# Kernel tuning notes

Measured on AMD Instinct MI355X. Metric: run time of the kernel, lower is better.

## Reference

```python
import jax, jax.numpy as jnp
import numpy as np

K = 256
ALPHA = 0.2   # bml_alpha
BETA = 0.3    # bml_beta
EPS = 1e-8    # torch CosineSimilarity eps
NEG_INF = -10000.0
WEIGHT_TEMP = 0.05


def _l2n(x):
    # cosine-normalize rows, matching nn.CosineSimilarity's eps clamp
    n = jnp.linalg.norm(x, axis=-1, keepdims=True)
    return x / jnp.maximum(n, EPS)


def setup_inputs() -> dict:
    key = jax.random.key(0)
    k1, k2, k3 = jax.random.split(key, 3)
    B, D = 8192, 768
    datapoints = jax.random.normal(k1, (B, D), dtype=jnp.float32)
    centroid = jax.random.normal(k2, (K, D), dtype=jnp.float32)
    batch_cos_sim = jax.random.normal(k3, (B, B), dtype=jnp.float32)
    return {"datapoints": datapoints, "centroid": centroid, "batch_cos_sim": batch_cos_sim}


def reference(datapoints, centroid, batch_cos_sim):
    B = datapoints.shape[0]
    datapoints = jax.lax.stop_gradient(datapoints)  # forward() does clone().detach()

    # intra_cos_sim = cos(datapoints, centroid) / temp (temp=1)  -> [B, K]
    intra_cos_sim = _l2n(datapoints) @ _l2n(centroid).T

    # cluster assignment + intra-class adjacency
    dp_index = jnp.argmax(intra_cos_sim, axis=-1)                 # [B]
    onehot = jax.nn.one_hot(dp_index, K, dtype=jnp.float32)       # [B, K]
    dp_cluster = onehot @ onehot.T                                # [B, B]
    eye = jnp.eye(B, dtype=bool)
    dp_cluster = jnp.where(eye, 0.0, dp_cluster)                  # fill_diagonal_(0)

    # gather assigned centroid per datapoint
    dp_centroid = centroid[dp_index]                              # [B, D]

    # hard negative: 2nd-closest centroid (top-2 on cosine sim), detached
    _, top2_idx = jax.lax.top_k(intra_cos_sim, 2)                 # [B, 2]
    hard_negative = jax.lax.stop_gradient(centroid[top2_idx[:, 1]])  # [B, D]

    # false-negative BML loss on the in-batch cosine matrix
    pos = jnp.diagonal(batch_cos_sim)[:, None]                    # [B, 1]
    delta = (batch_cos_sim - pos) * dp_cluster                    # [B, B]
    fn_loss = (jax.nn.relu(delta + ALPHA) + jax.nn.relu(-delta - BETA)).mean()

    # softmax-weighted negatives (diag masked to -10000), detached
    masked = jnp.where(eye, NEG_INF, batch_cos_sim)
    weights = jax.lax.stop_gradient(jax.nn.softmax(masked, axis=-1) / WEIGHT_TEMP)

    return intra_cos_sim, dp_cluster, dp_centroid, hard_negative, fn_loss, weights
```

## Files before the change

### kernel.cpp

```cpp
#include <hip/hip_runtime.h>
#include <math.h>

#define B_N 8192
#define K_N 256
#define D_N 768
#define BM 32
#define KC 32

static constexpr float ALPHA_C = 0.2f;
static constexpr float BETA_C  = 0.3f;
static constexpr float EPS_C   = 1e-8f;
static constexpr float NEG_INF_C = -10000.0f;
static constexpr float INV_WTEMP = 20.0f;

__global__ __launch_bounds__(256) void k_centroid_prep(
        const float* __restrict__ centroid, float* __restrict__ cnt) {
    int c = blockIdx.x, t = threadIdx.x;
    const float* p = centroid + c * D_N;
    float v0 = p[t], v1 = p[t + 256], v2 = p[t + 512];
    float s = v0 * v0 + v1 * v1 + v2 * v2;
    #pragma unroll
    for (int o = 32; o >= 1; o >>= 1) s += __shfl_xor(s, o);
    __shared__ float red[4];
    __shared__ float sinv;
    if ((t & 63) == 0) red[t >> 6] = s;
    __syncthreads();
    if (t == 0)
        sinv = 1.0f / fmaxf(sqrtf(red[0] + red[1] + red[2] + red[3]), EPS_C);
    __syncthreads();
    float inv = sinv;
    cnt[(t)       * K_N + c] = v0 * inv;
    cnt[(t + 256) * K_N + c] = v1 * inv;
    cnt[(t + 512) * K_N + c] = v2 * inv;
}

__device__ __forceinline__ bool top_better(float v, int iv, float w, int iw) {
    return (v > w) || ((v == w) && (iv < iw));
}

__global__ __launch_bounds__(256) void k_intra(
        const float* __restrict__ dp, const float* __restrict__ cnt,
        const float* __restrict__ centroid,
        float* __restrict__ out_intra, unsigned char* __restrict__ cid_g,
        float* __restrict__ dp_centroid, float* __restrict__ hard_negative) {
    __shared__ float ct[KC][K_N];
    __shared__ float dpt[KC][BM + 4];
    __shared__ float sqp[BM][8];
    __shared__ float rn[BM];
    int t = threadIdx.x;
    int row0 = blockIdx.x * BM;
    int tx = t & 63, ty = t >> 6;
    int c0 = tx * 4;
    int r0 = ty * 8;
    int sr = t >> 3, skq = t & 7;

    float acc[8][4];
    #pragma unroll
    for (int r = 0; r < 8; ++r)
        #pragma unroll
        for (int c = 0; c < 4; ++c) acc[r][c] = 0.f;
    float ss = 0.f;

    for (int kb = 0; kb < D_N; kb += KC) {
        __syncthreads();
        #pragma unroll
        for (int u = 0; u < 8; ++u) {
            int f4 = t + 256 * u;
            int k = f4 >> 6, c4 = (f4 & 63) << 2;
            *(float4*)&ct[k][c4] = *(const float4*)&cnt[(size_t)(kb + k) * K_N + c4];
        }
        {
            float4 v = *(const float4*)&dp[(size_t)(row0 + sr) * D_N + kb + skq * 4];
            ss += v.x * v.x + v.y * v.y + v.z * v.z + v.w * v.w;
            dpt[skq * 4 + 0][sr] = v.x;
            dpt[skq * 4 + 1][sr] = v.y;
            dpt[skq * 4 + 2][sr] = v.z;
            dpt[skq * 4 + 3][sr] = v.w;
        }
        __syncthreads();
        #pragma unroll
        for (int k = 0; k < KC; ++k) {
            float4 b4 = *(float4*)&ct[k][c0];
            float4 a0 = *(float4*)&dpt[k][r0];
            float4 a1 = *(float4*)&dpt[k][r0 + 4];
            float a[8] = {a0.x, a0.y, a0.z, a0.w, a1.x, a1.y, a1.z, a1.w};
            float b[4] = {b4.x, b4.y, b4.z, b4.w};
            #pragma unroll
            for (int r = 0; r < 8; ++r)
                #pragma unroll
                for (int c = 0; c < 4; ++c)
                    acc[r][c] += a[r] * b[c];
        }
    }

    sqp[sr][skq] = ss;
    __syncthreads();
    if (t < BM) {
        float s = 0.f;
        #pragma unroll
        for (int j = 0; j < 8; ++j) s += sqp[t][j];
        rn[t] = 1.0f / fmaxf(sqrtf(s), EPS_C);
    }
    __syncthreads();

    #pragma unroll 1
    for (int r = 0; r < 8; ++r) {
        int row = row0 + r0 + r;
        float rv = rn[r0 + r];
        float4 o;
        o.x = acc[r][0] * rv; o.y = acc[r][1] * rv;
        o.z = acc[r][2] * rv; o.w = acc[r][3] * rv;
        *(float4*)&out_intra[(size_t)row * K_N + c0] = o;

        float m1 = o.x, m2 = -1e30f;
        int i1 = c0, i2 = K_N;
        { float v = o.y; int id = c0 + 1;
          if (v > m1) { m2 = m1; i2 = i1; m1 = v; i1 = id; } else if (v > m2) { m2 = v; i2 = id; } }
        { float v = o.z; int id = c0 + 2;
          if (v > m1) { m2 = m1; i2 = i1; m1 = v; i1 = id; } else if (v > m2) { m2 = v; i2 = id; } }
        { float v = o.w; int id = c0 + 3;
          if (v > m1) { m2 = m1; i2 = i1; m1 = v; i1 = id; } else if (v > m2) { m2 = v; i2 = id; } }
        #pragma unroll
        for (int off = 32; off >= 1; off >>= 1) {
            float om1 = __shfl_xor(m1, off);
            int   oi1 = __shfl_xor(i1, off);
            float om2 = __shfl_xor(m2, off);
            int   oi2 = __shfl_xor(i2, off);
            if (top_better(om1, oi1, m1, i1)) {
                if (top_better(m1, i1, om2, oi2)) { m2 = m1; i2 = i1; }
                else                              { m2 = om2; i2 = oi2; }
                m1 = om1; i1 = oi1;
            } else if (top_better(om1, oi1, m2, i2)) {
                m2 = om1; i2 = oi1;
            }
        }
        if (tx == 0) cid_g[row] = (unsigned char)i1;

        const float4* s1 = (const float4*)(centroid + (size_t)i1 * D_N);
        const float4* s2 = (const float4*)(centroid + (size_t)i2 * D_N);
        float4* d1 = (float4*)(dp_centroid   + (size_t)row * D_N);
        float4* d2 = (float4*)(hard_negative + (size_t)row * D_N);
        #pragma unroll
        for (int u = 0; u < 3; ++u) {
            d1[tx + 64 * u] = s1[tx + 64 * u];
            d2[tx + 64 * u] = s2[tx + 64 * u];
        }
    }
}

__global__ __launch_bounds__(256) void k_row(
        const float* __restrict__ bcs, const unsigned char* __restrict__ cid_g,
        float* __restrict__ dp_cluster, float* __restrict__ weights,
        float* __restrict__ partials) {
    int i = blockIdx.x;
    int t = threadIdx.x;
    __shared__ float red_se[4], red_fn[4];
    __shared__ float posb;
    const unsigned* cidw = (const unsigned*)cid_g;

    const float4* src = (const float4*)(bcs + (size_t)i * B_N);
    float4 v[8];
    unsigned cw[8];
    #pragma unroll
    for (int u = 0; u < 8; ++u) {
        int f4 = t + 256 * u;
        v[u] = src[f4];
        cw[u] = cidw[f4];
    }
    {
        int ti = (i >> 2) & 255;
        int ui = i >> 10;
        int q  = i & 3;
        if (t == ti) {
            float pe = 0.f;
            #pragma unroll
            for (int u = 0; u < 8; ++u)
                if (u == ui)
                    pe = (q == 0) ? v[u].x : (q == 1) ? v[u].y
                       : (q == 2) ? v[u].z : v[u].w;
            posb = pe;
        }
    }
    __syncthreads();
    float pos = posb;
    unsigned myc = (unsigned)cid_g[i];

    float fn = 0.f, se = 0.f;
    float* dcrow = dp_cluster + (size_t)i * B_N;
    #pragma unroll
    for (int u = 0; u < 8; ++u) {
        int f4 = t + 256 * u;
        int j0 = f4 * 4;
        unsigned c = cw[u];
        float4 w = v[u], e, dc;
        {
            bool same = ((c & 255u) == myc) & (j0 != i);
            float delta = same ? (w.x - pos) : 0.f;
            fn += fmaxf(delta + ALPHA_C, 0.f) + fmaxf(-delta - BETA_C, 0.f);
            dc.x = same ? 1.0f : 0.f;
            e.x = __expf((j0 == i) ? NEG_INF_C : w.x);
        }
        {
            bool same = (((c >> 8) & 255u) == myc) & (j0 + 1 != i);
            float delta = same ? (w.y - pos) : 0.f;
            fn += fmaxf(delta + ALPHA_C, 0.f) + fmaxf(-delta - BETA_C, 0.f);
            dc.y = same ? 1.0f : 0.f;
            e.y = __expf((j0 + 1 == i) ? NEG_INF_C : w.y);
        }
        {
            bool same = (((c >> 16) & 255u) == myc) & (j0 + 2 != i);
            float delta = same ? (w.z - pos) : 0.f;
            fn += fmaxf(delta + ALPHA_C, 0.f) + fmaxf(-delta - BETA_C, 0.f);
            dc.z = same ? 1.0f : 0.f;
            e.z = __expf((j0 + 2 == i) ? NEG_INF_C : w.z);
        }
        {
            bool same = (((c >> 24) & 255u) == myc) & (j0 + 3 != i);
            float delta = same ? (w.w - pos) : 0.f;
            fn += fmaxf(delta + ALPHA_C, 0.f) + fmaxf(-delta - BETA_C, 0.f);
            dc.w = same ? 1.0f : 0.f;
            e.w = __expf((j0 + 3 == i) ? NEG_INF_C : w.w);
        }
        se += e.x + e.y + e.z + e.w;
        v[u] = e;
        ((float4*)dcrow)[f4] = dc;
    }

    #pragma unroll
    for (int o = 32; o >= 1; o >>= 1) {
        se += __shfl_xor(se, o);
        fn += __shfl_xor(fn, o);
    }
    if ((t & 63) == 0) { red_se[t >> 6] = se; red_fn[t >> 6] = fn; }
    __syncthreads();
    se = red_se[0] + red_se[1] + red_se[2] + red_se[3];
    float inv = INV_WTEMP / se;

    float* wrow = weights + (size_t)i * B_N;
    #pragma unroll
    for (int u = 0; u < 8; ++u) {
        int j0 = (t + 256 * u) * 4;
        wrow[j0]     = v[u].x * inv;
        wrow[j0 + 1] = v[u].y * inv;
        wrow[j0 + 2] = v[u].z * inv;
        wrow[j0 + 3] = v[u].w * inv;
    }

    if (t == 0)
        partials[i] = red_fn[0] + red_fn[1] + red_fn[2] + red_fn[3];
}

__global__ __launch_bounds__(256) void k_final(
        const float* __restrict__ partials, float* __restrict__ out) {
    int t = threadIdx.x;
    __shared__ double red[4];
    double s = 0.0;
    #pragma unroll
    for (int u = 0; u < 32; ++u) s += (double)partials[t + 256 * u];
    #pragma unroll
    for (int o = 32; o >= 1; o >>= 1) s += __shfl_xor(s, o);
    if ((t & 63) == 0) red[t >> 6] = s;
    __syncthreads();
    if (t == 0)
        out[0] = (float)((red[0] + red[1] + red[2] + red[3])
                         / ((double)B_N * (double)B_N));
}

extern "C" void kernel_launch(void* const* d_in, const int* in_sizes, int n_in,
                              void* d_out, int out_size, void* d_ws, size_t ws_size,
                              hipStream_t stream) {
    const float* dp       = (const float*)d_in[0];
    const float* centroid = (const float*)d_in[1];
    const float* bcs      = (const float*)d_in[2];
    float* out = (float*)d_out;

    float* intra       = out;
    float* dp_cluster  = out + 2097152;
    float* dp_centroid = out + 69206016;
    float* hard_neg    = out + 75497472;
    float* fn_out      = out + 81788928;
    float* weights     = out + 81788929;

    char* ws = (char*)d_ws;
    float*         cnt      = (float*)(ws + 256);
    unsigned char* cid      = (unsigned char*)(ws + 256 + 786432);
    float*         partials = (float*)(ws + 256 + 786432 + 8192);

    k_centroid_prep<<<K_N, 256, 0, stream>>>(centroid, cnt);
    k_intra<<<B_N / BM, 256, 0, stream>>>(dp, cnt, centroid, intra, cid,
                                          dp_centroid, hard_neg);
    k_row<<<B_N, 256, 0, stream>>>(bcs, cid, dp_cluster, weights, partials);
    k_final<<<1, 256, 0, stream>>>(partials, fn_out);
}
```

Measured before the change: 241.4 us.

## Process four rows per block in k_row with double-buffered row prefetch

Each k_row block now handles four consecutive rows instead of one. The cluster-id words are loaded once and reused across those rows, and the next row's 32 KB is prefetched into a second register buffer while the current row is processed. The diagonal positives are read directly from global memory instead of being broadcast through shared memory, and the fn partials shrink to one per block. This cuts the block count and redundant cid loads and adds memory-level parallelism, at the cost of doubled register use for row data and possibly lower occupancy.

```diff
diff --git a/kernel.cpp b/kernel.cpp
--- a/kernel.cpp
+++ b/kernel.cpp
@@ -6,6 +6,7 @@
 #define D_N 768
 #define BM 32
 #define KC 32
+#define RPB 4
 
 static constexpr float ALPHA_C = 0.2f;
 static constexpr float BETA_C  = 0.3f;
@@ -152,102 +153,95 @@
         const float* __restrict__ bcs, const unsigned char* __restrict__ cid_g,
         float* __restrict__ dp_cluster, float* __restrict__ weights,
         float* __restrict__ partials) {
-    int i = blockIdx.x;
+    int i0 = blockIdx.x * RPB;
     int t = threadIdx.x;
-    __shared__ float red_se[4], red_fn[4];
-    __shared__ float posb;
+    __shared__ float red_se[RPB][4];
+    __shared__ float red_fn[4];
     const unsigned* cidw = (const unsigned*)cid_g;
 
-    const float4* src = (const float4*)(bcs + (size_t)i * B_N);
-    float4 v[8];
+    unsigned mycw = cidw[i0 >> 2];
+    float pos0 = bcs[(size_t)(i0 + 0) * B_N + (i0 + 0)];
+    float pos1 = bcs[(size_t)(i0 + 1) * B_N + (i0 + 1)];
+    float pos2 = bcs[(size_t)(i0 + 2) * B_N + (i0 + 2)];
+    float pos3 = bcs[(size_t)(i0 + 3) * B_N + (i0 + 3)];
+
     unsigned cw[8];
     #pragma unroll
-    for (int u = 0; u < 8; ++u) {
-        int f4 = t + 256 * u;
-        v[u] = src[f4];
-        cw[u] = cidw[f4];
-    }
+    for (int u = 0; u < 8; ++u) cw[u] = cidw[t + 256 * u];
+
+    float4 va[8], vb[8];
     {
-        int ti = (i >> 2) & 255;
-        int ui = i >> 10;
-        int q  = i & 3;
-        if (t == ti) {
-            float pe = 0.f;
-            #pragma unroll
-            for (int u = 0; u < 8; ++u)
-                if (u == ui)
-                    pe = (q == 0) ? v[u].x : (q == 1) ? v[u].y
-                       : (q == 2) ? v[u].z : v[u].w;
-            posb = pe;
-        }
-    }
-    __syncthreads();
-    float pos = posb;
-    unsigned myc = (unsigned)cid_g[i];
-
-    float fn = 0.f, se = 0.f;
-    float* dcrow = dp_cluster + (size_t)i * B_N;
-    #pragma unroll
-    for (int u = 0; u < 8; ++u) {
-        int f4 = t + 256 * u;
-        int j0 = f4 * 4;
-        unsigned c = cw[u];
-        float4 w = v[u], e, dc;
-        {
-            bool same = ((c & 255u) == myc) & (j0 != i);
-            float delta = same ? (w.x - pos) : 0.f;
-            fn += fmaxf(delta + ALPHA_C, 0.f) + fmaxf(-delta - BETA_C, 0.f);
-            dc.x = same ? 1.0f : 0.f;
-            e.x = __expf((j0 == i) ? NEG_INF_C : w.x);
-        }
-        {
-            bool same = (((c >> 8) & 255u) == myc) & (j0 + 1 != i);
-            float delta = same ? (w.y - pos) : 0.f;
-            fn += fmaxf(delta + ALPHA_C, 0.f) + fmaxf(-delta - BETA_C, 0.f);
-            dc.y = same ? 1.0f : 0.f;
-            e.y = __expf((j0 + 1 == i) ? NEG_INF_C : w.y);
-        }
-        {
-            bool same = (((c >> 16) & 255u) == myc) & (j0 + 2 != i);
-            float delta = same ? (w.z - pos) : 0.f;
-            fn += fmaxf(delta + ALPHA_C, 0.f) + fmaxf(-delta - BETA_C, 0.f);
-            dc.z = same ? 1.0f : 0.f;
-            e.z = __expf((j0 + 2 == i) ? NEG_INF_C : w.z);
-        }
-        {
-            bool same = (((c >> 24) & 255u) == myc) & (j0 + 3 != i);
-            float delta = same ? (w.w - pos) : 0.f;
-            fn += fmaxf(delta + ALPHA_C, 0.f) + fmaxf(-delta - BETA_C, 0.f);
-            dc.w = same ? 1.0f : 0.f;
-            e.w = __expf((j0 + 3 == i) ? NEG_INF_C : w.w);
-        }
-        se += e.x + e.y + e.z + e.w;
-        v[u] = e;
-        ((float4*)dcrow)[f4] = dc;
-    }
-
-    #pragma unroll
-    for (int o = 32; o >= 1; o >>= 1) {
-        se += __shfl_xor(se, o);
-        fn += __shfl_xor(fn, o);
-    }
-    if ((t & 63) == 0) { red_se[t >> 6] = se; red_fn[t >> 6] = fn; }
-    __syncthreads();
-    se = red_se[0] + red_se[1] + red_se[2] + red_se[3];
-    float inv = INV_WTEMP / se;
-
-    float* wrow = weights + (size_t)i * B_N;
-    #pragma unroll
-    for (int u = 0; u < 8; ++u) {
-        int j0 = (t + 256 * u) * 4;
-        wrow[j0]     = v[u].x * inv;
-        wrow[j0 + 1] = v[u].y * inv;
-        wrow[j0 + 2] = v[u].z * inv;
-        wrow[j0 + 3] = v[u].w * inv;
-    }
-
+        const float4* s0 = (const float4*)(bcs + (size_t)i0 * B_N);
+        #pragma unroll
+        for (int u = 0; u < 8; ++u) va[u] = s0[t + 256 * u];
+    }
+
+    float fnacc = 0.f;
+
+#define ROW_PHASE(R, CUR, NXT, POS)                                            \
+    {                                                                          \
+        int i = i0 + R;                                                        \
+        if (R < RPB - 1) {                                                     \
+            const float4* sn = (const float4*)(bcs + (size_t)(i + 1) * B_N);   \
+            _Pragma("unroll")                                                  \
+            for (int u = 0; u < 8; ++u) NXT[u] = sn[t + 256 * u];              \
+        }                                                                      \
+        unsigned myc = (mycw >> (R * 8)) & 255u;                               \
+        float pos = POS;                                                       \
+        float fn = 0.f, se = 0.f;                                              \
+        float* dcrow = dp_cluster + (size_t)i * B_N;                           \
+        _Pragma("unroll")                                                      \
+        for (int u = 0; u < 8; ++u) {                                          \
+            int f4 = t + 256 * u; int j0 = f4 * 4; unsigned c = cw[u];         \
+            float4 w = CUR[u], e, dc;                                          \
+            bool b0 = ((c        & 255u) == myc) & (j0     != i);              \
+            bool b1 = (((c >> 8) & 255u) == myc) & (j0 + 1 != i);              \
+            bool b2 = (((c >> 16)& 255u) == myc) & (j0 + 2 != i);              \
+            bool b3 = (((c >> 24)& 255u) == myc) & (j0 + 3 != i);              \
+            float d0 = b0 ? (w.x - pos) : 0.f, d1 = b1 ? (w.y - pos) : 0.f;    \
+            float d2 = b2 ? (w.z - pos) : 0.f, d3 = b3 ? (w.w - pos) : 0.f;    \
+            fn += fmaxf(d0 + ALPHA_C, 0.f) + fmaxf(-d0 - BETA_C, 0.f);         \
+            fn += fmaxf(d1 + ALPHA_C, 0.f) + fmaxf(-d1 - BETA_C, 0.f);         \
+            fn += fmaxf(d2 + ALPHA_C, 0.f) + fmaxf(-d2 - BETA_C, 0.f);         \
+            fn += fmaxf(d3 + ALPHA_C, 0.f) + fmaxf(-d3 - BETA_C, 0.f);         \
+            dc.x = b0 ? 1.f : 0.f; dc.y = b1 ? 1.f : 0.f;                      \
+            dc.z = b2 ? 1.f : 0.f; dc.w = b3 ? 1.f : 0.f;                      \
+            e.x = __expf((j0     == i) ? NEG_INF_C : w.x);                     \
+            e.y = __expf((j0 + 1 == i) ? NEG_INF_C : w.y);                     \
+            e.z = __expf((j0 + 2 == i) ? NEG_INF_C : w.z);                     \
+            e.w = __expf((j0 + 3 == i) ? NEG_INF_C : w.w);                     \
+            se += e.x + e.y + e.z + e.w;                                       \
+            CUR[u] = e;                                                        \
+            ((float4*)dcrow)[f4] = dc;                                         \
+        }                                                                      \
+        fnacc += fn;                                                           \
+        _Pragma("unroll")                                                      \
+        for (int o = 32; o >= 1; o >>= 1) se += __shfl_xor(se, o);             \
+        if ((t & 63) == 0) red_se[R][t >> 6] = se;                             \
+        __syncthreads();                                                       \
+        se = red_se[R][0] + red_se[R][1] + red_se[R][2] + red_se[R][3];        \
+        float inv = INV_WTEMP / se;                                            \
+        float* wrow = weights + (size_t)i * B_N;                               \
+        _Pragma("unroll")                                                      \
+        for (int u = 0; u < 8; ++u) {                                          \
+            int j0 = (t + 256 * u) * 4;                                        \
+            wrow[j0]     = CUR[u].x * inv; wrow[j0 + 1] = CUR[u].y * inv;      \
+            wrow[j0 + 2] = CUR[u].z * inv; wrow[j0 + 3] = CUR[u].w * inv;      \
+        }                                                                      \
+    }
+
+    ROW_PHASE(0, va, vb, pos0)
+    ROW_PHASE(1, vb, va, pos1)
+    ROW_PHASE(2, va, vb, pos2)
+    ROW_PHASE(3, vb, va, pos3)
+#undef ROW_PHASE
+
+    #pragma unroll
+    for (int o = 32; o >= 1; o >>= 1) fnacc += __shfl_xor(fnacc, o);
+    if ((t & 63) == 0) red_fn[t >> 6] = fnacc;
+    __syncthreads();
     if (t == 0)
-        partials[i] = red_fn[0] + red_fn[1] + red_fn[2] + red_fn[3];
+        partials[blockIdx.x] = red_fn[0] + red_fn[1] + red_fn[2] + red_fn[3];
 }
 
 __global__ __launch_bounds__(256) void k_final(
@@ -256,7 +250,7 @@
     __shared__ double red[4];
     double s = 0.0;
     #pragma unroll
-    for (int u = 0; u < 32; ++u) s += (double)partials[t + 256 * u];
+    for (int u = 0; u < 8; ++u) s += (double)partials[t + 256 * u];
     #pragma unroll
     for (int o = 32; o >= 1; o >>= 1) s += __shfl_xor(s, o);
     if ((t & 63) == 0) red[t >> 6] = s;
@@ -289,6 +283,6 @@
     k_centroid_prep<<<K_N, 256, 0, stream>>>(centroid, cnt);
     k_intra<<<B_N / BM, 256, 0, stream>>>(dp, cnt, centroid, intra, cid,
                                           dp_centroid, hard_neg);
-    k_row<<<B_N, 256, 0, stream>>>(bcs, cid, dp_cluster, weights, partials);
+    k_row<<<B_N / RPB, 256, 0, stream>>>(bcs, cid, dp_cluster, weights, partials);
     k_final<<<1, 256, 0, stream>>>(partials, fn_out);
 }
```

New measurement: 245.6 us. About the same (+1.7%).
